# Optimization experiments

Hardware: AMD Instinct MI355X
Metric: run time of the kernel (lower is better)

The kernel has to match this reference:

```python
import jax, jax.numpy as jnp
import numpy as np

N_NODES = 50000
N_PAIRS = 625000
F = 128

def setup_inputs() -> dict:
    key = jax.random.key(0)
    k1, k2, k3, k4, k5 = jax.random.split(key, 5)
    x = jax.random.normal(k1, (N_NODES, F), dtype=jnp.float32)
    alpha_ij = jax.random.normal(k2, (N_PAIRS,), dtype=jnp.float32)
    idx_i = jax.random.randint(k3, (N_PAIRS,), 0, N_NODES, dtype=jnp.int32)
    idx_j = jax.random.randint(k4, (N_PAIRS,), 0, N_NODES, dtype=jnp.int32)
    # Dense(F, use_bias=False) kernel, shape (F_in, F_out)
    W = jax.random.normal(k5, (F, F), dtype=jnp.float32) / np.sqrt(F)
    return {"x": x, "alpha_ij": alpha_ij, "idx_i": idx_i, "idx_j": idx_j, "W": W}

def reference(x, alpha_ij, idx_i, idx_j, W):
    # dense projection on nodes (n,F) @ (F,F) -> (n,F)
    v = jnp.matmul(x, W)
    # gather neighbor values, scale by attention coeff: (n_pairs, F)
    msg = alpha_ij[:, None] * v[idx_j]
    # scatter-sum back to center atoms
    return jax.ops.segment_sum(msg, segment_ids=idx_i, num_segments=x.shape[0])
```

## Files before the change

kernel.cpp:

```cpp
#include <hip/hip_runtime.h>
#include <stdint.h>

#define FDIM 128
#define BR 64
#define SLOTS 48
#define NB_C 196
#define QC 4096
#define PPB 2048
#define P2SPLIT 8

typedef short  s8v   __attribute__((ext_vector_type(8)));
typedef float  f4v   __attribute__((ext_vector_type(4)));
typedef unsigned short u8v __attribute__((ext_vector_type(8)));

__device__ __forceinline__ unsigned short f2bf(float f) {
    union { float f; uint32_t u; } c; c.f = f;
    uint32_t u = c.u;
    return (unsigned short)((u + 0x7fffu + ((u >> 16) & 1u)) >> 16);
}
__device__ __forceinline__ float bflo2f(uint32_t g) {
    union { uint32_t u; float f; } c; c.u = g << 16; return c.f;
}
__device__ __forceinline__ float bfhi2f(uint32_t g) {
    union { uint32_t u; float f; } c; c.u = g & 0xffff0000u; return c.f;
}

__global__ __launch_bounds__(256) void prep(const float* __restrict__ W,
                                            unsigned short* __restrict__ Wt,
                                            int* __restrict__ cnt,
                                            int* __restrict__ gcur,
                                            int n_nodes) {
    int i = blockIdx.x * 256 + threadIdx.x;
    if (i < FDIM * FDIM) {
        int n = i & 127, k = i >> 7;
        Wt[n * FDIM + k] = f2bf(W[k * FDIM + n]);
    }
    if (i < n_nodes) cnt[i] = 0;
    if (i < NB_C)    gcur[i] = 0;
}

__global__ __launch_bounds__(256) void fused_gemm_pass1(
        const float* __restrict__ x,
        const unsigned short* __restrict__ Wt,
        unsigned short* __restrict__ v,
        const int* __restrict__ idx_i,
        const int* __restrict__ idx_j,
        const float* __restrict__ alpha,
        int* __restrict__ gcur,
        unsigned long long* __restrict__ qrec,
        int n_rows, int n_pairs, int PB) {
    __shared__ unsigned short As[BR][FDIM + 8];

    if ((int)blockIdx.x < PB) {
        __shared__ int hist[NB_C];
        __shared__ int base_s[NB_C];
        const int t = threadIdx.x;
        const int start = blockIdx.x * PPB;

        if (t < NB_C) hist[t] = 0;
        __syncthreads();

        unsigned long long rec[8];
        int bkt[8];
#pragma unroll
        for (int i = 0; i < 8; ++i) {
            int p = start + t + i * 256;
            bkt[i] = -1;
            if (p < n_pairs) {
                int ii = idx_i[p];
                int b  = ii >> 8;
                bkt[i] = b;
                rec[i] = (unsigned long long)(uint32_t)(idx_j[p] | ((ii & 255) << 16) | (b << 24))
                       | ((unsigned long long)(uint32_t)__float_as_int(alpha[p]) << 32);
                atomicAdd(&hist[b], 1);
            }
        }
        __syncthreads();
        if (t < NB_C) {
            int h = hist[t];
            base_s[t] = (h > 0) ? atomicAdd(&gcur[t], h) : 0;
            hist[t] = 0;
        }
        __syncthreads();
#pragma unroll
        for (int i = 0; i < 8; ++i) {
            int b = bkt[i];
            if (b >= 0) {
                int lp  = atomicAdd(&hist[b], 1);
                int pos = base_s[b] + lp;
                if (pos < QC)
                    qrec[(size_t)b * QC + pos] = rec[i];
            }
        }
        return;
    }

    const int t = threadIdx.x;
    const int row0 = (blockIdx.x - PB) * BR;
    {
        int r  = t >> 2;
        int c0 = (t & 3) * 32;
        int grow = row0 + r;
        const float* src = x + (size_t)grow * FDIM + c0;
#pragma unroll
        for (int it = 0; it < 4; ++it) {
            float4 xa = make_float4(0.f, 0.f, 0.f, 0.f);
            float4 xb = make_float4(0.f, 0.f, 0.f, 0.f);
            if (grow < n_rows) {
                xa = *(const float4*)(src + it * 8);
                xb = *(const float4*)(src + it * 8 + 4);
            }
            u8v pk;
            pk[0] = f2bf(xa.x); pk[1] = f2bf(xa.y); pk[2] = f2bf(xa.z); pk[3] = f2bf(xa.w);
            pk[4] = f2bf(xb.x); pk[5] = f2bf(xb.y); pk[6] = f2bf(xb.z); pk[7] = f2bf(xb.w);
            *(u8v*)(&As[r][c0 + it * 8]) = pk;
        }
    }
    __syncthreads();

    const int w    = t >> 6;
    const int lane = t & 63;
    const int rt   = (w & 1) * 32;
    const int ct   = (w >> 1) * 64;
    const int lrow = lane & 15;
    const int kq   = (lane >> 4) * 8;

    f4v acc[2][4];
#pragma unroll
    for (int i = 0; i < 2; ++i)
#pragma unroll
        for (int j = 0; j < 4; ++j)
            acc[i][j] = (f4v){0.f, 0.f, 0.f, 0.f};

#pragma unroll
    for (int ks = 0; ks < 4; ++ks) {
        const int k0 = ks * 32 + kq;
        const unsigned short* wb = Wt + (size_t)(ct + lrow) * FDIM + k0;
        s8v b0 = *(const s8v*)(wb);
        s8v b1 = *(const s8v*)(wb + 16 * FDIM);
        s8v b2 = *(const s8v*)(wb + 32 * FDIM);
        s8v b3 = *(const s8v*)(wb + 48 * FDIM);
        s8v a0 = *(const s8v*)(&As[rt + lrow][k0]);
        s8v a1 = *(const s8v*)(&As[rt + 16 + lrow][k0]);
        acc[0][0] = __builtin_amdgcn_mfma_f32_16x16x32_bf16(a0, b0, acc[0][0], 0, 0, 0);
        acc[0][1] = __builtin_amdgcn_mfma_f32_16x16x32_bf16(a0, b1, acc[0][1], 0, 0, 0);
        acc[0][2] = __builtin_amdgcn_mfma_f32_16x16x32_bf16(a0, b2, acc[0][2], 0, 0, 0);
        acc[0][3] = __builtin_amdgcn_mfma_f32_16x16x32_bf16(a0, b3, acc[0][3], 0, 0, 0);
        acc[1][0] = __builtin_amdgcn_mfma_f32_16x16x32_bf16(a1, b0, acc[1][0], 0, 0, 0);
        acc[1][1] = __builtin_amdgcn_mfma_f32_16x16x32_bf16(a1, b1, acc[1][1], 0, 0, 0);
        acc[1][2] = __builtin_amdgcn_mfma_f32_16x16x32_bf16(a1, b2, acc[1][2], 0, 0, 0);
        acc[1][3] = __builtin_amdgcn_mfma_f32_16x16x32_bf16(a1, b3, acc[1][3], 0, 0, 0);
    }

    const int quad = lane >> 4;
#pragma unroll
    for (int i = 0; i < 2; ++i) {
#pragma unroll
        for (int r = 0; r < 4; ++r) {
            int row = row0 + rt + i * 16 + quad * 4 + r;
            if (row < n_rows) {
#pragma unroll
                for (int j = 0; j < 4; ++j) {
                    int col = ct + j * 16 + lrow;
                    v[(size_t)row * FDIM + col] = f2bf(acc[i][j][r]);
                }
            }
        }
    }
}

__global__ __launch_bounds__(256) void pass2(const unsigned long long* __restrict__ qrec,
                                             const int* __restrict__ gcur,
                                             int* __restrict__ cnt,
                                             int2* __restrict__ pairs) {
    const int c    = blockIdx.x / P2SPLIT;
    const int part = blockIdx.x % P2SPLIT;
    int nrec = gcur[c];
    nrec = (nrec > QC) ? QC : nrec;
    const int lo = (nrec * part) / P2SPLIT;
    const int hi = (nrec * (part + 1)) / P2SPLIT;
    const unsigned long long* q = qrec + (size_t)c * QC;

    for (int k = lo + threadIdx.x; k < hi; k += 256) {
        unsigned long long r = q[k];
        uint32_t lowb = (uint32_t)r;
        int j    = lowb & 0xffff;
        int node = c * 256 + ((lowb >> 16) & 0xff);
        int pos  = atomicAdd(&cnt[node], 1);
        if (pos < SLOTS) {
            int2 pr;
            pr.x = j;
            pr.y = (int)(r >> 32);
            pairs[(size_t)node * SLOTS + pos] = pr;
        }
    }
}

__global__ __launch_bounds__(256) void aggregate(const unsigned short* __restrict__ v,
                                                 const int* __restrict__ cnt,
                                                 const int2* __restrict__ pairs,
                                                 float* __restrict__ out,
                                                 int n_nodes) {
    const int node = blockIdx.x * 4 + (threadIdx.x >> 6);
    const int lane = threadIdx.x & 63;
    if (node >= n_nodes) return;

    int deg = cnt[node];
    deg = (deg > SLOTS) ? SLOTS : deg;
    const int2* pp = pairs + (size_t)node * SLOTS;

    float ax = 0.f, ay = 0.f;
    int k = 0;
    for (; k + 4 <= deg; k += 4) {
        int4 q0 = *(const int4*)(pp + k);
        int4 q1 = *(const int4*)(pp + k + 2);
        float a0 = __int_as_float(q0.y);
        float a1 = __int_as_float(q0.w);
        float a2 = __int_as_float(q1.y);
        float a3 = __int_as_float(q1.w);
        uint32_t g0 = *(const uint32_t*)(v + (size_t)q0.x * FDIM + lane * 2);
        uint32_t g1 = *(const uint32_t*)(v + (size_t)q0.z * FDIM + lane * 2);
        uint32_t g2 = *(const uint32_t*)(v + (size_t)q1.x * FDIM + lane * 2);
        uint32_t g3 = *(const uint32_t*)(v + (size_t)q1.z * FDIM + lane * 2);
        ax += a0 * bflo2f(g0) + a1 * bflo2f(g1);
        ay += a0 * bfhi2f(g0) + a1 * bfhi2f(g1);
        ax += a2 * bflo2f(g2) + a3 * bflo2f(g3);
        ay += a2 * bfhi2f(g2) + a3 * bfhi2f(g3);
    }
    if (k + 2 <= deg) {
        int4 q0 = *(const int4*)(pp + k);
        float a0 = __int_as_float(q0.y);
        float a1 = __int_as_float(q0.w);
        uint32_t g0 = *(const uint32_t*)(v + (size_t)q0.x * FDIM + lane * 2);
        uint32_t g1 = *(const uint32_t*)(v + (size_t)q0.z * FDIM + lane * 2);
        ax += a0 * bflo2f(g0) + a1 * bflo2f(g1);
        ay += a0 * bfhi2f(g0) + a1 * bfhi2f(g1);
        k += 2;
    }
    if (k < deg) {
        int2 p0 = pp[k];
        float a0 = __int_as_float(p0.y);
        uint32_t g0 = *(const uint32_t*)(v + (size_t)p0.x * FDIM + lane * 2);
        ax += a0 * bflo2f(g0);
        ay += a0 * bfhi2f(g0);
    }
    float2 r;
    r.x = ax;
    r.y = ay;
    *(float2*)(out + (size_t)node * FDIM + lane * 2) = r;
}

extern "C" void kernel_launch(void* const* d_in, const int* in_sizes, int n_in,
                              void* d_out, int out_size, void* d_ws, size_t ws_size,
                              hipStream_t stream) {
    const float* x     = (const float*)d_in[0];
    const float* alpha = (const float*)d_in[1];
    const int*   idx_i = (const int*)d_in[2];
    const int*   idx_j = (const int*)d_in[3];
    const float* W     = (const float*)d_in[4];

    const int n_nodes = in_sizes[0] / FDIM;
    const int n_pairs = in_sizes[1];

    char* ws = (char*)d_ws;
    size_t off = 0;
    auto carve = [&](size_t bytes) {
        char* p = ws + off;
        off += (bytes + 255) & ~(size_t)255;
        return p;
    };
    unsigned short* v  = (unsigned short*)carve((size_t)n_nodes * FDIM * sizeof(unsigned short));
    unsigned short* Wt = (unsigned short*)carve((size_t)FDIM * FDIM * sizeof(unsigned short));
    int*  cnt  = (int*)carve((size_t)n_nodes * sizeof(int));
    int*  gcur = (int*)carve((size_t)NB_C * sizeof(int));
    unsigned long long* qrec =
        (unsigned long long*)carve((size_t)NB_C * QC * sizeof(unsigned long long));
    int2* pairs = (int2*)carve((size_t)n_nodes * SLOTS * sizeof(int2));
    float* out  = (float*)d_out;

    int pb = (max(n_nodes, FDIM * FDIM) + 255) / 256;
    prep<<<pb, 256, 0, stream>>>(W, Wt, cnt, gcur, n_nodes);

    int GB = (n_nodes + BR - 1) / BR;
    int PB = (n_pairs + PPB - 1) / PPB;
    fused_gemm_pass1<<<PB + GB, 256, 0, stream>>>(x, Wt, v, idx_i, idx_j, alpha,
                                                  gcur, qrec, n_nodes, n_pairs, PB);

    pass2<<<NB_C * P2SPLIT, 256, 0, stream>>>(qrec, gcur, cnt, pairs);

    int ablocks = (n_nodes + 3) / 4;
    aggregate<<<ablocks, 256, 0, stream>>>(v, cnt, pairs, out, n_nodes);
}
```

Measured before the change: 151.0 us.

## Enlarge bucketing chunks, re-read inputs in scatter pass, unroll aggregate by eight

Each bucketing block now processes 8192 pairs instead of 2048. It no longer keeps records in registers between the histogram and scatter phases; it re-reads idx_i, idx_j and alpha in the second phase. This cuts the number of blocks and the global atomics on the bucket cursors, but costs extra global reads and lowers parallelism in that phase. The aggregate kernel's main loop is unrolled to eight neighbours so more independent gathers are in flight per iteration, with a four-neighbour tail added.

Result: slower. 162.1 us (+7.4%).

```diff
diff --git a/kernel.cpp b/kernel.cpp
--- a/kernel.cpp
+++ b/kernel.cpp
@@ -6,7 +6,7 @@
 #define SLOTS 48
 #define NB_C 196
 #define QC 4096
-#define PPB 2048
+#define PPB 8192
 #define P2SPLIT 8
 
 typedef short  s8v   __attribute__((ext_vector_type(8)));
@@ -60,36 +60,34 @@
         if (t < NB_C) hist[t] = 0;
         __syncthreads();
 
-        unsigned long long rec[8];
-        int bkt[8];
-#pragma unroll
-        for (int i = 0; i < 8; ++i) {
+#pragma unroll 4
+        for (int i = 0; i < 32; ++i) {
             int p = start + t + i * 256;
-            bkt[i] = -1;
-            if (p < n_pairs) {
-                int ii = idx_i[p];
-                int b  = ii >> 8;
-                bkt[i] = b;
-                rec[i] = (unsigned long long)(uint32_t)(idx_j[p] | ((ii & 255) << 16) | (b << 24))
-                       | ((unsigned long long)(uint32_t)__float_as_int(alpha[p]) << 32);
-                atomicAdd(&hist[b], 1);
-            }
+            if (p < n_pairs)
+                atomicAdd(&hist[idx_i[p] >> 8], 1);
         }
         __syncthreads();
+
         if (t < NB_C) {
             int h = hist[t];
             base_s[t] = (h > 0) ? atomicAdd(&gcur[t], h) : 0;
             hist[t] = 0;
         }
         __syncthreads();
-#pragma unroll
-        for (int i = 0; i < 8; ++i) {
-            int b = bkt[i];
-            if (b >= 0) {
+
+#pragma unroll 4
+        for (int i = 0; i < 32; ++i) {
+            int p = start + t + i * 256;
+            if (p < n_pairs) {
+                int ii = idx_i[p];
+                int b  = ii >> 8;
+                unsigned long long rec =
+                    (unsigned long long)(uint32_t)(idx_j[p] | ((ii & 255) << 16))
+                  | ((unsigned long long)(uint32_t)__float_as_int(alpha[p]) << 32);
                 int lp  = atomicAdd(&hist[b], 1);
                 int pos = base_s[b] + lp;
                 if (pos < QC)
-                    qrec[(size_t)b * QC + pos] = rec[i];
+                    qrec[(size_t)b * QC + pos] = rec;
             }
         }
         return;
@@ -184,12 +182,11 @@
     for (int k = lo + threadIdx.x; k < hi; k += 256) {
         unsigned long long r = q[k];
         uint32_t lowb = (uint32_t)r;
-        int j    = lowb & 0xffff;
         int node = c * 256 + ((lowb >> 16) & 0xff);
         int pos  = atomicAdd(&cnt[node], 1);
         if (pos < SLOTS) {
             int2 pr;
-            pr.x = j;
+            pr.x = lowb & 0xffff;
             pr.y = (int)(r >> 32);
             pairs[(size_t)node * SLOTS + pos] = pr;
         }
@@ -211,13 +208,37 @@
 
     float ax = 0.f, ay = 0.f;
     int k = 0;
-    for (; k + 4 <= deg; k += 4) {
+    for (; k + 8 <= deg; k += 8) {
         int4 q0 = *(const int4*)(pp + k);
         int4 q1 = *(const int4*)(pp + k + 2);
-        float a0 = __int_as_float(q0.y);
-        float a1 = __int_as_float(q0.w);
-        float a2 = __int_as_float(q1.y);
-        float a3 = __int_as_float(q1.w);
+        int4 q2 = *(const int4*)(pp + k + 4);
+        int4 q3 = *(const int4*)(pp + k + 6);
+        uint32_t g0 = *(const uint32_t*)(v + (size_t)q0.x * FDIM + lane * 2);
+        uint32_t g1 = *(const uint32_t*)(v + (size_t)q0.z * FDIM + lane * 2);
+        uint32_t g2 = *(const uint32_t*)(v + (size_t)q1.x * FDIM + lane * 2);
+        uint32_t g3 = *(const uint32_t*)(v + (size_t)q1.z * FDIM + lane * 2);
+        uint32_t g4 = *(const uint32_t*)(v + (size_t)q2.x * FDIM + lane * 2);
+        uint32_t g5 = *(const uint32_t*)(v + (size_t)q2.z * FDIM + lane * 2);
+        uint32_t g6 = *(const uint32_t*)(v + (size_t)q3.x * FDIM + lane * 2);
+        uint32_t g7 = *(const uint32_t*)(v + (size_t)q3.z * FDIM + lane * 2);
+        float a0 = __int_as_float(q0.y), a1 = __int_as_float(q0.w);
+        float a2 = __int_as_float(q1.y), a3 = __int_as_float(q1.w);
+        float a4 = __int_as_float(q2.y), a5 = __int_as_float(q2.w);
+        float a6 = __int_as_float(q3.y), a7 = __int_as_float(q3.w);
+        ax += a0 * bflo2f(g0) + a1 * bflo2f(g1);
+        ay += a0 * bfhi2f(g0) + a1 * bfhi2f(g1);
+        ax += a2 * bflo2f(g2) + a3 * bflo2f(g3);
+        ay += a2 * bfhi2f(g2) + a3 * bfhi2f(g3);
+        ax += a4 * bflo2f(g4) + a5 * bflo2f(g5);
+        ay += a4 * bfhi2f(g4) + a5 * bfhi2f(g5);
+        ax += a6 * bflo2f(g6) + a7 * bflo2f(g7);
+        ay += a6 * bfhi2f(g6) + a7 * bfhi2f(g7);
+    }
+    if (k + 4 <= deg) {
+        int4 q0 = *(const int4*)(pp + k);
+        int4 q1 = *(const int4*)(pp + k + 2);
+        float a0 = __int_as_float(q0.y), a1 = __int_as_float(q0.w);
+        float a2 = __int_as_float(q1.y), a3 = __int_as_float(q1.w);
         uint32_t g0 = *(const uint32_t*)(v + (size_t)q0.x * FDIM + lane * 2);
         uint32_t g1 = *(const uint32_t*)(v + (size_t)q0.z * FDIM + lane * 2);
         uint32_t g2 = *(const uint32_t*)(v + (size_t)q1.x * FDIM + lane * 2);
@@ -226,11 +247,11 @@
         ay += a0 * bfhi2f(g0) + a1 * bfhi2f(g1);
         ax += a2 * bflo2f(g2) + a3 * bflo2f(g3);
         ay += a2 * bfhi2f(g2) + a3 * bfhi2f(g3);
+        k += 4;
     }
     if (k + 2 <= deg) {
         int4 q0 = *(const int4*)(pp + k);
-        float a0 = __int_as_float(q0.y);
-        float a1 = __int_as_float(q0.w);
+        float a0 = __int_as_float(q0.y), a1 = __int_as_float(q0.w);
         uint32_t g0 = *(const uint32_t*)(v + (size_t)q0.x * FDIM + lane * 2);
         uint32_t g1 = *(const uint32_t*)(v + (size_t)q0.z * FDIM + lane * 2);
         ax += a0 * bflo2f(g0) + a1 * bflo2f(g1);
```

## Fuse per-node binning and aggregation into one bucket-level LDS sort kernel

Applied to the files above, without the earlier changes.

Replaces the global pass2 scatter into fixed per-node slot arrays plus the separate aggregate kernel with a single kernel. Each block owns one 256-node bucket, counting-sorts its records in shared memory, and then has each wavefront aggregate 16 nodes. This removes the global cnt and pairs round trip, the global atomics, the cnt zeroing in prep, and one launch. In exchange it runs only 196 blocks of 1024 threads with 64KB of LDS, so parallelism and occupancy during the gather phase are much lower. It also drops the SLOTS degree cap.

Result: faster. 140.2 us (median of 2 runs) (-7.1%).

```diff
diff --git a/kernel.cpp b/kernel.cpp
--- a/kernel.cpp
+++ b/kernel.cpp
@@ -3,11 +3,9 @@
 
 #define FDIM 128
 #define BR 64
-#define SLOTS 48
 #define NB_C 196
 #define QC 4096
 #define PPB 2048
-#define P2SPLIT 8
 
 typedef short  s8v   __attribute__((ext_vector_type(8)));
 typedef float  f4v   __attribute__((ext_vector_type(4)));
@@ -27,16 +25,13 @@
 
 __global__ __launch_bounds__(256) void prep(const float* __restrict__ W,
                                             unsigned short* __restrict__ Wt,
-                                            int* __restrict__ cnt,
-                                            int* __restrict__ gcur,
-                                            int n_nodes) {
+                                            int* __restrict__ gcur) {
     int i = blockIdx.x * 256 + threadIdx.x;
     if (i < FDIM * FDIM) {
         int n = i & 127, k = i >> 7;
         Wt[n * FDIM + k] = f2bf(W[k * FDIM + n]);
     }
-    if (i < n_nodes) cnt[i] = 0;
-    if (i < NB_C)    gcur[i] = 0;
+    if (i < NB_C) gcur[i] = 0;
 }
 
 __global__ __launch_bounds__(256) void fused_gemm_pass1(
@@ -70,7 +65,7 @@
                 int ii = idx_i[p];
                 int b  = ii >> 8;
                 bkt[i] = b;
-                rec[i] = (unsigned long long)(uint32_t)(idx_j[p] | ((ii & 255) << 16) | (b << 24))
+                rec[i] = (unsigned long long)(uint32_t)(idx_j[p] | ((ii & 255) << 16))
                        | ((unsigned long long)(uint32_t)__float_as_int(alpha[p]) << 32);
                 atomicAdd(&hist[b], 1);
             }
@@ -169,85 +164,116 @@
     }
 }
 
-__global__ __launch_bounds__(256) void pass2(const unsigned long long* __restrict__ qrec,
-                                             const int* __restrict__ gcur,
-                                             int* __restrict__ cnt,
-                                             int2* __restrict__ pairs) {
-    const int c    = blockIdx.x / P2SPLIT;
-    const int part = blockIdx.x % P2SPLIT;
+__global__ __launch_bounds__(1024) void bucket_agg(
+        const unsigned short* __restrict__ v,
+        const int* __restrict__ gcur,
+        const unsigned long long* __restrict__ qrec,
+        float* __restrict__ out,
+        int n_nodes) {
+    __shared__ unsigned long long sraw[QC];
+    __shared__ unsigned long long ssort[QC];
+    __shared__ int cnt256[256];
+    __shared__ int scanbuf[256];
+    __shared__ int start[257];
+    const int t = threadIdx.x;
+    const int c = blockIdx.x;
+
     int nrec = gcur[c];
     nrec = (nrec > QC) ? QC : nrec;
-    const int lo = (nrec * part) / P2SPLIT;
-    const int hi = (nrec * (part + 1)) / P2SPLIT;
     const unsigned long long* q = qrec + (size_t)c * QC;
 
-    for (int k = lo + threadIdx.x; k < hi; k += 256) {
+    if (t < 256) cnt256[t] = 0;
+    __syncthreads();
+    for (int k = t; k < nrec; k += 1024) {
         unsigned long long r = q[k];
-        uint32_t lowb = (uint32_t)r;
-        int j    = lowb & 0xffff;
-        int node = c * 256 + ((lowb >> 16) & 0xff);
-        int pos  = atomicAdd(&cnt[node], 1);
-        if (pos < SLOTS) {
-            int2 pr;
-            pr.x = j;
-            pr.y = (int)(r >> 32);
-            pairs[(size_t)node * SLOTS + pos] = pr;
-        }
-    }
-}
-
-__global__ __launch_bounds__(256) void aggregate(const unsigned short* __restrict__ v,
-                                                 const int* __restrict__ cnt,
-                                                 const int2* __restrict__ pairs,
-                                                 float* __restrict__ out,
-                                                 int n_nodes) {
-    const int node = blockIdx.x * 4 + (threadIdx.x >> 6);
-    const int lane = threadIdx.x & 63;
-    if (node >= n_nodes) return;
-
-    int deg = cnt[node];
-    deg = (deg > SLOTS) ? SLOTS : deg;
-    const int2* pp = pairs + (size_t)node * SLOTS;
-
-    float ax = 0.f, ay = 0.f;
-    int k = 0;
-    for (; k + 4 <= deg; k += 4) {
-        int4 q0 = *(const int4*)(pp + k);
-        int4 q1 = *(const int4*)(pp + k + 2);
-        float a0 = __int_as_float(q0.y);
-        float a1 = __int_as_float(q0.w);
-        float a2 = __int_as_float(q1.y);
-        float a3 = __int_as_float(q1.w);
-        uint32_t g0 = *(const uint32_t*)(v + (size_t)q0.x * FDIM + lane * 2);
-        uint32_t g1 = *(const uint32_t*)(v + (size_t)q0.z * FDIM + lane * 2);
-        uint32_t g2 = *(const uint32_t*)(v + (size_t)q1.x * FDIM + lane * 2);
-        uint32_t g3 = *(const uint32_t*)(v + (size_t)q1.z * FDIM + lane * 2);
-        ax += a0 * bflo2f(g0) + a1 * bflo2f(g1);
-        ay += a0 * bfhi2f(g0) + a1 * bfhi2f(g1);
-        ax += a2 * bflo2f(g2) + a3 * bflo2f(g3);
-        ay += a2 * bfhi2f(g2) + a3 * bfhi2f(g3);
-    }
-    if (k + 2 <= deg) {
-        int4 q0 = *(const int4*)(pp + k);
-        float a0 = __int_as_float(q0.y);
-        float a1 = __int_as_float(q0.w);
-        uint32_t g0 = *(const uint32_t*)(v + (size_t)q0.x * FDIM + lane * 2);
-        uint32_t g1 = *(const uint32_t*)(v + (size_t)q0.z * FDIM + lane * 2);
-        ax += a0 * bflo2f(g0) + a1 * bflo2f(g1);
-        ay += a0 * bfhi2f(g0) + a1 * bfhi2f(g1);
-        k += 2;
-    }
-    if (k < deg) {
-        int2 p0 = pp[k];
-        float a0 = __int_as_float(p0.y);
-        uint32_t g0 = *(const uint32_t*)(v + (size_t)p0.x * FDIM + lane * 2);
-        ax += a0 * bflo2f(g0);
-        ay += a0 * bfhi2f(g0);
-    }
-    float2 r;
-    r.x = ax;
-    r.y = ay;
-    *(float2*)(out + (size_t)node * FDIM + lane * 2) = r;
+        sraw[k] = r;
+        atomicAdd(&cnt256[(int)((r >> 16) & 0xff)], 1);
+    }
+    __syncthreads();
+
+    if (t < 256) scanbuf[t] = cnt256[t];
+    __syncthreads();
+    for (int d = 1; d < 256; d <<= 1) {
+        int tmp = 0;
+        if (t < 256 && t >= d) tmp = scanbuf[t - d];
+        __syncthreads();
+        if (t < 256) scanbuf[t] += tmp;
+        __syncthreads();
+    }
+    if (t < 256) {
+        int excl = scanbuf[t] - cnt256[t];
+        start[t]  = excl;
+        cnt256[t] = excl;
+    }
+    if (t == 0) start[256] = scanbuf[255];
+    __syncthreads();
+
+    for (int k = t; k < nrec; k += 1024) {
+        unsigned long long r = sraw[k];
+        int off = (int)((r >> 16) & 0xff);
+        int pos = atomicAdd(&cnt256[off], 1);
+        ssort[pos] = r;
+    }
+    __syncthreads();
+
+    const int wv   = t >> 6;
+    const int lane = t & 63;
+#pragma unroll 1
+    for (int i = 0; i < 16; ++i) {
+        const int off  = wv * 16 + i;
+        const int node = c * 256 + off;
+        const int s0 = start[off];
+        const int s1 = start[off + 1];
+
+        float ax = 0.f, ay = 0.f;
+        int k = s0;
+        for (; k + 4 <= s1; k += 4) {
+            unsigned long long r0 = ssort[k];
+            unsigned long long r1 = ssort[k + 1];
+            unsigned long long r2 = ssort[k + 2];
+            unsigned long long r3 = ssort[k + 3];
+            int j0 = (int)(r0 & 0xffff), j1 = (int)(r1 & 0xffff);
+            int j2 = (int)(r2 & 0xffff), j3 = (int)(r3 & 0xffff);
+            float a0 = __int_as_float((int)(r0 >> 32));
+            float a1 = __int_as_float((int)(r1 >> 32));
+            float a2 = __int_as_float((int)(r2 >> 32));
+            float a3 = __int_as_float((int)(r3 >> 32));
+            uint32_t g0 = *(const uint32_t*)(v + (size_t)j0 * FDIM + lane * 2);
+            uint32_t g1 = *(const uint32_t*)(v + (size_t)j1 * FDIM + lane * 2);
+            uint32_t g2 = *(const uint32_t*)(v + (size_t)j2 * FDIM + lane * 2);
+            uint32_t g3 = *(const uint32_t*)(v + (size_t)j3 * FDIM + lane * 2);
+            ax += a0 * bflo2f(g0) + a1 * bflo2f(g1);
+            ay += a0 * bfhi2f(g0) + a1 * bfhi2f(g1);
+            ax += a2 * bflo2f(g2) + a3 * bflo2f(g3);
+            ay += a2 * bfhi2f(g2) + a3 * bfhi2f(g3);
+        }
+        if (k + 2 <= s1) {
+            unsigned long long r0 = ssort[k];
+            unsigned long long r1 = ssort[k + 1];
+            int j0 = (int)(r0 & 0xffff), j1 = (int)(r1 & 0xffff);
+            float a0 = __int_as_float((int)(r0 >> 32));
+            float a1 = __int_as_float((int)(r1 >> 32));
+            uint32_t g0 = *(const uint32_t*)(v + (size_t)j0 * FDIM + lane * 2);
+            uint32_t g1 = *(const uint32_t*)(v + (size_t)j1 * FDIM + lane * 2);
+            ax += a0 * bflo2f(g0) + a1 * bflo2f(g1);
+            ay += a0 * bfhi2f(g0) + a1 * bfhi2f(g1);
+            k += 2;
+        }
+        if (k < s1) {
+            unsigned long long r0 = ssort[k];
+            int j0 = (int)(r0 & 0xffff);
+            float a0 = __int_as_float((int)(r0 >> 32));
+            uint32_t g0 = *(const uint32_t*)(v + (size_t)j0 * FDIM + lane * 2);
+            ax += a0 * bflo2f(g0);
+            ay += a0 * bfhi2f(g0);
+        }
+        if (node < n_nodes) {
+            float2 r;
+            r.x = ax;
+            r.y = ay;
+            *(float2*)(out + (size_t)node * FDIM + lane * 2) = r;
+        }
+    }
 }
 
 extern "C" void kernel_launch(void* const* d_in, const int* in_sizes, int n_in,
@@ -271,23 +297,17 @@
     };
     unsigned short* v  = (unsigned short*)carve((size_t)n_nodes * FDIM * sizeof(unsigned short));
     unsigned short* Wt = (unsigned short*)carve((size_t)FDIM * FDIM * sizeof(unsigned short));
-    int*  cnt  = (int*)carve((size_t)n_nodes * sizeof(int));
     int*  gcur = (int*)carve((size_t)NB_C * sizeof(int));
     unsigned long long* qrec =
         (unsigned long long*)carve((size_t)NB_C * QC * sizeof(unsigned long long));
-    int2* pairs = (int2*)carve((size_t)n_nodes * SLOTS * sizeof(int2));
-    float* out  = (float*)d_out;
-
-    int pb = (max(n_nodes, FDIM * FDIM) + 255) / 256;
-    prep<<<pb, 256, 0, stream>>>(W, Wt, cnt, gcur, n_nodes);
+    float* out = (float*)d_out;
+
+    prep<<<(FDIM * FDIM + 255) / 256, 256, 0, stream>>>(W, Wt, gcur);
 
     int GB = (n_nodes + BR - 1) / BR;
     int PB = (n_pairs + PPB - 1) / PPB;
     fused_gemm_pass1<<<PB + GB, 256, 0, stream>>>(x, Wt, v, idx_i, idx_j, alpha,
                                                   gcur, qrec, n_nodes, n_pairs, PB);
 
-    pass2<<<NB_C * P2SPLIT, 256, 0, stream>>>(qrec, gcur, cnt, pairs);
-
-    int ablocks = (n_nodes + 3) / 4;
-    aggregate<<<ablocks, 256, 0, stream>>>(v, cnt, pairs, out, n_nodes);
-}
+    bucket_agg<<<NB_C, 1024, 0, stream>>>(v, gcur, qrec, out, n_nodes);
+}
```
